# Performance work log

Hardware: AMD Instinct MI355X
Metric: run time of the kernel (lower is better)

The kernel has to match this reference:

```python
import jax, jax.numpy as jnp
import numpy as np

N_CELL = 66
N_SUB = 29934
N = N_CELL + N_SUB  # 30000 nodes
F = 256
E_HALF = 480000
K = 3
LAYERS = 2
BN_EPS = 1e-5


def setup_inputs() -> dict:
    key = jax.random.key(0)
    ks = jax.random.split(key, 8)
    cell_feat = jax.random.normal(ks[0], (N_CELL, F), dtype=jnp.float32)
    sub_feat = jax.random.normal(ks[1], (N_SUB, F), dtype=jnp.float32)
    # interaction_edge builds a symmetric directed edge list: (a,b) and (b,a)
    src = jax.random.randint(ks[2], (E_HALF,), 0, N)
    dst = jax.random.randint(ks[3], (E_HALF,), 0, N)
    edge_index = jnp.stack([jnp.concatenate([src, dst]),
                            jnp.concatenate([dst, src])], axis=0)
    ew_half = jax.random.uniform(ks[4], (E_HALF,), dtype=jnp.float32, minval=0.1, maxval=1.0)
    edge_weight = jnp.concatenate([ew_half, ew_half])
    glorot = np.sqrt(6.0 / (F + F))
    W1 = jax.random.uniform(ks[5], (F, F), dtype=jnp.float32, minval=-glorot, maxval=glorot)
    W2 = jax.random.uniform(ks[6], (F, F), dtype=jnp.float32, minval=-glorot, maxval=glorot)
    b1 = jnp.zeros((F,), jnp.float32)
    b2 = jnp.zeros((F,), jnp.float32)
    prelu_w = jnp.full((F,), 0.25, jnp.float32)  # PReLU default init
    gamma = jnp.ones((F,), jnp.float32)
    beta = jnp.zeros((F,), jnp.float32)
    return {"cell_feat": cell_feat, "sub_feat": sub_feat,
            "edge_index": edge_index, "edge_weight": edge_weight,
            "W1": W1, "b1": b1, "W2": W2, "b2": b2,
            "prelu_w": prelu_w, "gamma": gamma, "beta": beta}


def _gcn_norm(edge_index, edge_weight, n):
    # SGConv's gcn_norm: add self-loops (weight 1), symmetric degree normalization
    loop = jnp.arange(n)
    row = jnp.concatenate([edge_index[0], loop])  # source j
    col = jnp.concatenate([edge_index[1], loop])  # target i
    ew = jnp.concatenate([edge_weight, jnp.ones((n,), edge_weight.dtype)])
    deg = jax.ops.segment_sum(ew, col, num_segments=n)
    dinv = jnp.where(deg > 0, jax.lax.rsqrt(deg), 0.0)
    norm = dinv[row] * ew * dinv[col]
    return row, col, norm


def _sgconv(x, row, col, norm, W, b, n):
    # K-hop propagation: x <- A_hat^K x, then linear
    for _ in range(K):
        x = jax.ops.segment_sum(norm[:, None] * x[row], col, num_segments=n)
    return x @ W.T + b


def _prelu_bn(x, prelu_w, gamma, beta):
    x = jnp.where(x >= 0, x, prelu_w * x)
    mean = jnp.mean(x, axis=0)
    var = jnp.mean(jnp.square(x - mean), axis=0)  # biased, training-mode BN
    return gamma * (x - mean) * jax.lax.rsqrt(var + BN_EPS) + beta


def reference(cell_feat, sub_feat, edge_index, edge_weight,
              W1, b1, W2, b2, prelu_w, gamma, beta):
    x = jnp.concatenate([cell_feat, sub_feat], axis=0)  # [N, F]
    n = x.shape[0]
    row, col, norm = _gcn_norm(edge_index, edge_weight, n)
    for W, b in ((W1, b1), (W2, b2)):
        x = _sgconv(x, row, col, norm, W, b, n)
        x = _prelu_bn(x, prelu_w, gamma, beta)
    return x[:N_CELL, :], x[N_CELL:, :]
```

## Files before the change

kernel.cpp:

```cpp
#include <hip/hip_runtime.h>
#include <hip/hip_bf16.h>

constexpr int NN    = 30000;
constexpr int NCELL = 66;
constexpr int NF    = 256;
constexpr int CAP   = 80;
constexpr float EPS = 1e-5f;

using bf16x8 = __attribute__((ext_vector_type(8))) short;
using f32x4  = __attribute__((ext_vector_type(4))) float;
using f32x2  = __attribute__((ext_vector_type(2))) float;

__device__ __forceinline__ float bf2f(unsigned short u) {
    return __uint_as_float(((unsigned)u) << 16);
}
__device__ __forceinline__ unsigned short f2bf(float f) {
    __hip_bfloat16 h = __float2bfloat16(f);
    return *reinterpret_cast<unsigned short*>(&h);
}
__device__ __forceinline__ void acc8v(f32x2* acc, float4 u, float w) {
    unsigned a = __float_as_uint(u.x), b = __float_as_uint(u.y);
    unsigned c = __float_as_uint(u.z), d = __float_as_uint(u.w);
    f32x2 wv; wv[0] = w; wv[1] = w;
    f32x2 e0; e0[0] = __uint_as_float(a << 16); e0[1] = __uint_as_float(a & 0xffff0000u);
    f32x2 e1; e1[0] = __uint_as_float(b << 16); e1[1] = __uint_as_float(b & 0xffff0000u);
    f32x2 e2; e2[0] = __uint_as_float(c << 16); e2[1] = __uint_as_float(c & 0xffff0000u);
    f32x2 e3; e3[0] = __uint_as_float(d << 16); e3[1] = __uint_as_float(d & 0xffff0000u);
    acc[0] += wv * e0;
    acc[1] += wv * e1;
    acc[2] += wv * e2;
    acc[3] += wv * e3;
}
__device__ __forceinline__ void acc8(float* acc, float4 u, float w) {
    unsigned a = __float_as_uint(u.x), b = __float_as_uint(u.y);
    unsigned c = __float_as_uint(u.z), d = __float_as_uint(u.w);
    acc[0] += w * __uint_as_float(a << 16);
    acc[1] += w * __uint_as_float(a & 0xffff0000u);
    acc[2] += w * __uint_as_float(b << 16);
    acc[3] += w * __uint_as_float(b & 0xffff0000u);
    acc[4] += w * __uint_as_float(c << 16);
    acc[5] += w * __uint_as_float(c & 0xffff0000u);
    acc[6] += w * __uint_as_float(d << 16);
    acc[7] += w * __uint_as_float(d & 0xffff0000u);
}
__device__ __forceinline__ void edge_meta(const unsigned* p, int& r, float& w) {
    unsigned v = *p;
    r = (int)(v & 0xffffu);
    w = (float)(v >> 16) * (1.0f / 65536.0f);
}

__global__ void k_init(int* fill, float* sums) {
    int i = blockIdx.x * 256 + threadIdx.x;
    if (i < NN) fill[i] = 0;
    if (i < 2 * NF) sums[i] = 0.0f;
}

__global__ void k_zero_stats(float* sums) {
    int i = threadIdx.x;
    if (i < 2 * NF) sums[i] = 0.0f;
}

__global__ void k_cvtw(const float4* __restrict__ W, ushort4* __restrict__ Wh) {
    int idx = blockIdx.x * 256 + threadIdx.x;
    if (idx >= NF * NF / 4) return;
    float4 v = W[idx];
    ushort4 o;
    o.x = f2bf(v.x); o.y = f2bf(v.y); o.z = f2bf(v.z); o.w = f2bf(v.w);
    Wh[idx] = o;
}

__global__ void k_scatter(const int* __restrict__ ei, const float* __restrict__ ew,
                          int* fill, unsigned* __restrict__ bkt, int E) {
    int e = blockIdx.x * 256 + threadIdx.x;
    if (e >= E) return;
    int row = ei[e];
    int col = ei[E + e];
    unsigned q = (unsigned)(ew[e] * 65536.0f);
    int pos = atomicAdd(&fill[col], 1);
    unsigned v = ((unsigned)row) | (q << 16);
    __builtin_nontemporal_store(v, &bkt[(size_t)col * CAP + pos]);
}

__global__ void k_deg(const unsigned* __restrict__ bkt, const int* __restrict__ fill,
                      float* __restrict__ s1, float* __restrict__ s2) {
    int i = blockIdx.x * 256 + threadIdx.x;
    if (i >= NN) return;
    int cnt = fill[i];
    unsigned sq = 0;
    const unsigned* p = bkt + (size_t)i * CAP;
    for (int e = 0; e < cnt; e++) sq += (p[e] >> 16);
    float deg = 1.0f + (float)sq * (1.0f / 65536.0f);
    float di = rsqrtf(deg);
    s2[i] = di;
    s1[i] = di * di;
}

__global__ void k_concat_h(const float4* __restrict__ cell, const float4* __restrict__ sub,
                           const float* __restrict__ dinv, ushort4* __restrict__ xh) {
    int idx = blockIdx.x * 256 + threadIdx.x;
    if (idx >= NN * (NF / 4)) return;
    const int CELL4 = NCELL * (NF / 4);
    float4 v = (idx < CELL4) ? cell[idx] : sub[idx - CELL4];
    float di = dinv[idx >> 6];
    ushort4 o;
    o.x = f2bf(v.x * di); o.y = f2bf(v.y * di);
    o.z = f2bf(v.z * di); o.w = f2bf(v.w * di);
    xh[idx] = o;
}

__global__ __launch_bounds__(256) void k_prop(const ushort* __restrict__ xin,
                                              ushort* __restrict__ xout,
                                              const int* __restrict__ fill,
                                              const unsigned* __restrict__ bkt,
                                              const float* __restrict__ scale) {
    int n = blockIdx.x * 4 + (threadIdx.x >> 6);
    int lane = threadIdx.x & 63;
    int half = lane >> 5;
    int fb = lane & 31;
    const float4* xrow = (const float4*)xin;
    const unsigned* base = bkt + (size_t)n * CAP;
    int cnt = fill[n];
    float4 uself = xrow[n * 32 + fb];
    float sc = scale[n];
    f32x2 acc[4];
    #pragma unroll
    for (int i = 0; i < 4; i++) { acc[i][0] = 0.f; acc[i][1] = 0.f; }
    int steps = cnt >> 1;
    int it = 0;
    int e = half;
    if (8 <= steps) {
        unsigned m[8];
        #pragma unroll
        for (int j = 0; j < 8; j++) m[j] = base[e + 2 * j];
        for (;;) {
            int   r[8];
            float w[8];
            #pragma unroll
            for (int j = 0; j < 8; j++) {
                r[j] = (int)(m[j] & 0xffffu);
                w[j] = (float)(m[j] >> 16) * (1.0f / 65536.0f);
            }
            float4 u[8];
            #pragma unroll
            for (int j = 0; j < 8; j++) u[j] = xrow[r[j] * 32 + fb];
            it += 8; e += 16;
            bool more = (it + 8 <= steps);
            if (more) {
                #pragma unroll
                for (int j = 0; j < 8; j++) m[j] = base[e + 2 * j];
            }
            #pragma unroll
            for (int j = 0; j < 8; j++) acc8v(acc, u[j], w[j]);
            if (!more) break;
        }
    }
    for (; it + 4 <= steps; it += 4, e += 8) {
        int r0, r1, r2, r3; float w0, w1, w2, w3;
        edge_meta(base + e,     r0, w0);
        edge_meta(base + e + 2, r1, w1);
        edge_meta(base + e + 4, r2, w2);
        edge_meta(base + e + 6, r3, w3);
        float4 u0 = xrow[r0 * 32 + fb];
        float4 u1 = xrow[r1 * 32 + fb];
        float4 u2 = xrow[r2 * 32 + fb];
        float4 u3 = xrow[r3 * 32 + fb];
        acc8v(acc, u0, w0); acc8v(acc, u1, w1); acc8v(acc, u2, w2); acc8v(acc, u3, w3);
    }
    for (; it < steps; ++it, e += 2) {
        int r0; float w0;
        edge_meta(base + e, r0, w0);
        float4 u0 = xrow[r0 * 32 + fb];
        acc8v(acc, u0, w0);
    }
    if ((cnt & 1) && half == 0) {
        int r0; float w0;
        edge_meta(base + cnt - 1, r0, w0);
        float4 u0 = xrow[r0 * 32 + fb];
        acc8v(acc, u0, w0);
    }
    float accs[8];
    #pragma unroll
    for (int i = 0; i < 4; i++) { accs[2 * i] = acc[i][0]; accs[2 * i + 1] = acc[i][1]; }
    #pragma unroll
    for (int i = 0; i < 8; i++) accs[i] += __shfl_xor(accs[i], 32);
    if (half == 0) {
        acc8(accs, uself, 1.0f);
        #pragma unroll
        for (int i = 0; i < 8; i++) accs[i] *= sc;
        unsigned p0 = ((unsigned)f2bf(accs[1]) << 16) | f2bf(accs[0]);
        unsigned p1 = ((unsigned)f2bf(accs[3]) << 16) | f2bf(accs[2]);
        unsigned p2 = ((unsigned)f2bf(accs[5]) << 16) | f2bf(accs[4]);
        unsigned p3 = ((unsigned)f2bf(accs[7]) << 16) | f2bf(accs[6]);
        float4 o;
        o.x = __uint_as_float(p0); o.y = __uint_as_float(p1);
        o.z = __uint_as_float(p2); o.w = __uint_as_float(p3);
        ((float4*)xout)[n * 32 + fb] = o;
    }
}

__global__ __launch_bounds__(256) void k_gemm_fused(const short* __restrict__ A,
                                                    const short* __restrict__ B,
                                                    const float* __restrict__ bias,
                                                    const float* __restrict__ pw,
                                                    float* __restrict__ y,
                                                    float* __restrict__ sums) {
    constexpr int RT = NN / 16;
    int w    = threadIdx.x >> 6;
    int lane = threadIdx.x & 63;
    int rt   = blockIdx.x * 4 + w;
    int ml   = lane & 15;
    int q    = lane >> 4;
    bool valid = rt < RT;
    __shared__ float red[2][4][NF];
    f32x4 acc[16];
    #pragma unroll
    for (int i = 0; i < 16; i++) acc[i] = (f32x4){0.f, 0.f, 0.f, 0.f};
    if (valid) {
        const short* arow = A + (rt * 16 + ml) * NF + q * 8;
        #pragma unroll
        for (int ks = 0; ks < 8; ks++) {
            bf16x8 a = *(const bf16x8*)(arow + ks * 32);
            #pragma unroll
            for (int nt = 0; nt < 16; nt++) {
                bf16x8 b = *(const bf16x8*)(B + (nt * 16 + ml) * NF + ks * 32 + q * 8);
                acc[nt] = __builtin_amdgcn_mfma_f32_16x16x32_bf16(a, b, acc[nt], 0, 0, 0);
            }
        }
    }
    #pragma unroll
    for (int nt = 0; nt < 16; nt++) {
        int col = nt * 16 + ml;
        float s = 0.f, s2 = 0.f;
        if (valid) {
            float bb = bias[col];
            float pc = pw[col];
            #pragma unroll
            for (int r = 0; r < 4; r++) {
                float v = acc[nt][r] + bb;
                v = (v >= 0.f) ? v : pc * v;
                s += v; s2 += v * v;
                y[(rt * 16 + q * 4 + r) * NF + col] = v;
            }
        }
        s  += __shfl_xor(s, 16);  s  += __shfl_xor(s, 32);
        s2 += __shfl_xor(s2, 16); s2 += __shfl_xor(s2, 32);
        if (lane < 16) { red[0][w][col] = s; red[1][w][col] = s2; }
    }
    __syncthreads();
    int t = threadIdx.x;
    float v0 = red[0][0][t] + red[0][1][t] + red[0][2][t] + red[0][3][t];
    float v1 = red[1][0][t] + red[1][1][t] + red[1][2][t] + red[1][3][t];
    atomicAdd(&sums[t], v0);
    atomicAdd(&sums[NF + t], v1);
}

__global__ void k_finalize(const float* __restrict__ sums, const float* __restrict__ gamma,
                           const float* __restrict__ beta, float* __restrict__ ss) {
    int t = threadIdx.x;
    float mean = sums[t] / (float)NN;
    float var = sums[NF + t] / (float)NN - mean * mean;
    if (var < 0.f) var = 0.f;
    float istd = rsqrtf(var + EPS);
    float sc = gamma[t] * istd;
    ss[t] = sc;
    ss[NF + t] = beta[t] - mean * sc;
}

__global__ void k_apply_h(const float4* __restrict__ y, const float* __restrict__ ss,
                          const float* __restrict__ dinv, ushort4* __restrict__ xh) {
    int idx = blockIdx.x * 256 + threadIdx.x;
    if (idx >= NN * (NF / 4)) return;
    int f = (idx & 63) * 4;
    float di = dinv[idx >> 6];
    float4 v = y[idx];
    ushort4 o;
    o.x = f2bf((v.x * ss[f]     + ss[NF + f])     * di);
    o.y = f2bf((v.y * ss[f + 1] + ss[NF + f + 1]) * di);
    o.z = f2bf((v.z * ss[f + 2] + ss[NF + f + 2]) * di);
    o.w = f2bf((v.w * ss[f + 3] + ss[NF + f + 3]) * di);
    xh[idx] = o;
}

__global__ void k_apply_out(const float4* __restrict__ y, const float* __restrict__ ss,
                            float4* __restrict__ out) {
    int idx = blockIdx.x * 256 + threadIdx.x;
    if (idx >= NN * (NF / 4)) return;
    int f = (idx & 63) * 4;
    float4 v = y[idx];
    float4 o;
    o.x = v.x * ss[f]     + ss[NF + f];
    o.y = v.y * ss[f + 1] + ss[NF + f + 1];
    o.z = v.z * ss[f + 2] + ss[NF + f + 2];
    o.w = v.w * ss[f + 3] + ss[NF + f + 3];
    out[idx] = o;
}

extern "C" void kernel_launch(void* const* d_in, const int* in_sizes, int n_in,
                              void* d_out, int out_size, void* d_ws, size_t ws_size,
                              hipStream_t stream) {
    const float* cell  = (const float*)d_in[0];
    const float* sub   = (const float*)d_in[1];
    const int*   ei    = (const int*)  d_in[2];
    const float* ew    = (const float*)d_in[3];
    const float* W1    = (const float*)d_in[4];
    const float* bias1 = (const float*)d_in[5];
    const float* W2    = (const float*)d_in[6];
    const float* bias2 = (const float*)d_in[7];
    const float* pw    = (const float*)d_in[8];
    const float* gamma = (const float*)d_in[9];
    const float* beta  = (const float*)d_in[10];
    float* out = (float*)d_out;
    const int E = in_sizes[3];

    char* ws = (char*)d_ws;
    size_t off = 0;
    auto alloc = [&](size_t bytes) -> void* {
        void* p = ws + off;
        off = (off + bytes + 255) & ~((size_t)255);
        return p;
    };
    ushort*   xh0  = (ushort*)  alloc((size_t)NN * NF * 2);
    ushort*   xh1  = (ushort*)  alloc((size_t)NN * NF * 2);
    float*    yf   = (float*)   alloc((size_t)NN * NF * 4);
    ushort*   W1h  = (ushort*)  alloc((size_t)NF * NF * 2);
    ushort*   W2h  = (ushort*)  alloc((size_t)NF * NF * 2);
    unsigned* bkt  = (unsigned*)alloc((size_t)NN * CAP * 4);
    int*      fill = (int*)     alloc((size_t)NN * 4);
    float*    s1   = (float*)   alloc((size_t)NN * 4);
    float*    s2   = (float*)   alloc((size_t)NN * 4);
    float*    sums = (float*)   alloc((size_t)2 * NF * 4);
    float*    ss   = (float*)   alloc((size_t)2 * NF * 4);

    const int gN  = (NN + 255) / 256;
    const int gE  = (E + 255) / 256;
    const int gV4 = (NN * NF / 4 + 255) / 256;
    const int gW4 = (NF * NF / 4 + 255) / 256;
    const int gP  = NN / 4;
    const int gG  = (NN / 16 + 3) / 4;

    k_init<<<gN, 256, 0, stream>>>(fill, sums);
    k_cvtw<<<gW4, 256, 0, stream>>>((const float4*)W1, (ushort4*)W1h);
    k_cvtw<<<gW4, 256, 0, stream>>>((const float4*)W2, (ushort4*)W2h);
    k_scatter<<<gE, 256, 0, stream>>>(ei, ew, fill, bkt, E);
    k_deg<<<gN, 256, 0, stream>>>(bkt, fill, s1, s2);
    k_concat_h<<<gV4, 256, 0, stream>>>((const float4*)cell, (const float4*)sub, s2, (ushort4*)xh0);

    k_prop<<<gP, 256, 0, stream>>>(xh0, xh1, fill, bkt, s1);
    k_prop<<<gP, 256, 0, stream>>>(xh1, xh0, fill, bkt, s1);
    k_prop<<<gP, 256, 0, stream>>>(xh0, xh1, fill, bkt, s2);
    k_gemm_fused<<<gG, 256, 0, stream>>>((const short*)xh1, (const short*)W1h, bias1, pw, yf, sums);
    k_finalize<<<1, 256, 0, stream>>>(sums, gamma, beta, ss);
    k_apply_h<<<gV4, 256, 0, stream>>>((const float4*)yf, ss, s2, (ushort4*)xh0);
    k_zero_stats<<<1, 512, 0, stream>>>(sums);

    k_prop<<<gP, 256, 0, stream>>>(xh0, xh1, fill, bkt, s1);
    k_prop<<<gP, 256, 0, stream>>>(xh1, xh0, fill, bkt, s1);
    k_prop<<<gP, 256, 0, stream>>>(xh0, xh1, fill, bkt, s2);
    k_gemm_fused<<<gG, 256, 0, stream>>>((const short*)xh1, (const short*)W2h, bias2, pw, yf, sums);
    k_finalize<<<1, 256, 0, stream>>>(sums, gamma, beta, ss);
    k_apply_out<<<gV4, 256, 0, stream>>>((const float4*)yf, ss, (float4*)out);
}
```

Measured before the change: 654.0 us.

## Merge setup kernels, partition edge scatter by destination range, fold BN finalize

After: 624.2 us. -4.6%, faster.

```diff
diff --git a/kernel.cpp b/kernel.cpp
--- a/kernel.cpp
+++ b/kernel.cpp
@@ -11,9 +11,6 @@
 using f32x4  = __attribute__((ext_vector_type(4))) float;
 using f32x2  = __attribute__((ext_vector_type(2))) float;
 
-__device__ __forceinline__ float bf2f(unsigned short u) {
-    return __uint_as_float(((unsigned)u) << 16);
-}
 __device__ __forceinline__ unsigned short f2bf(float f) {
     __hip_bfloat16 h = __float2bfloat16(f);
     return *reinterpret_cast<unsigned short*>(&h);
@@ -48,11 +45,35 @@
     r = (int)(v & 0xffffu);
     w = (float)(v >> 16) * (1.0f / 65536.0f);
 }
-
-__global__ void k_init(int* fill, float* sums) {
-    int i = blockIdx.x * 256 + threadIdx.x;
-    if (i < NN) fill[i] = 0;
-    if (i < 2 * NF) sums[i] = 0.0f;
+__device__ __forceinline__ void bn_ss(const float* sums, const float* gamma,
+                                      const float* beta, int col, float& sc, float& sh) {
+    float mean = sums[col] * (1.0f / (float)NN);
+    float var  = sums[NF + col] * (1.0f / (float)NN) - mean * mean;
+    if (var < 0.f) var = 0.f;
+    float istd = rsqrtf(var + EPS);
+    sc = gamma[col] * istd;
+    sh = beta[col] - mean * sc;
+}
+
+__global__ void k_setup(int* fill, float* sums,
+                        const float4* __restrict__ W1, ushort4* __restrict__ W1h,
+                        const float4* __restrict__ W2, ushort4* __restrict__ W2h) {
+    int b = blockIdx.x;
+    if (b < 118) {
+        int i = b * 256 + threadIdx.x;
+        if (i < NN) fill[i] = 0;
+        if (i < 2 * NF) sums[i] = 0.0f;
+    } else {
+        const float4* src = (b < 182) ? W1 : W2;
+        ushort4* dst      = (b < 182) ? W1h : W2h;
+        int idx = (b - ((b < 182) ? 118 : 182)) * 256 + threadIdx.x;
+        if (idx < NF * NF / 4) {
+            float4 v = src[idx];
+            ushort4 o;
+            o.x = f2bf(v.x); o.y = f2bf(v.y); o.z = f2bf(v.z); o.w = f2bf(v.w);
+            dst[idx] = o;
+        }
+    }
 }
 
 __global__ void k_zero_stats(float* sums) {
@@ -60,25 +81,27 @@
     if (i < 2 * NF) sums[i] = 0.0f;
 }
 
-__global__ void k_cvtw(const float4* __restrict__ W, ushort4* __restrict__ Wh) {
-    int idx = blockIdx.x * 256 + threadIdx.x;
-    if (idx >= NF * NF / 4) return;
-    float4 v = W[idx];
-    ushort4 o;
-    o.x = f2bf(v.x); o.y = f2bf(v.y); o.z = f2bf(v.z); o.w = f2bf(v.w);
-    Wh[idx] = o;
-}
-
-__global__ void k_scatter(const int* __restrict__ ei, const float* __restrict__ ew,
-                          int* fill, unsigned* __restrict__ bkt, int E) {
-    int e = blockIdx.x * 256 + threadIdx.x;
-    if (e >= E) return;
-    int row = ei[e];
-    int col = ei[E + e];
-    unsigned q = (unsigned)(ew[e] * 65536.0f);
-    int pos = atomicAdd(&fill[col], 1);
-    unsigned v = ((unsigned)row) | (q << 16);
-    __builtin_nontemporal_store(v, &bkt[(size_t)col * CAP + pos]);
+constexpr int SLICE = 2048;
+__global__ __launch_bounds__(256) void k_scatter8(const int* __restrict__ ei,
+                                                  const float* __restrict__ ew,
+                                                  int* fill, unsigned* __restrict__ bkt,
+                                                  int E) {
+    int r  = blockIdx.x & 7;
+    int s  = blockIdx.x >> 3;
+    int lo = r * (NN / 8);
+    int hi = lo + (NN / 8);
+    int e0 = s * SLICE;
+    int e1 = e0 + SLICE; if (e1 > E) e1 = E;
+    for (int e = e0 + threadIdx.x; e < e1; e += 256) {
+        int col = ei[E + e];
+        if (col >= lo && col < hi) {
+            int row  = ei[e];
+            float wv = ew[e];
+            unsigned q = (unsigned)(wv * 65536.0f);
+            int pos = atomicAdd(&fill[col], 1);
+            bkt[(size_t)col * CAP + pos] = ((unsigned)row) | (q << 16);
+        }
+    }
 }
 
 __global__ void k_deg(const unsigned* __restrict__ bkt, const int* __restrict__ fill,
@@ -254,44 +277,44 @@
     atomicAdd(&sums[NF + t], v1);
 }
 
-__global__ void k_finalize(const float* __restrict__ sums, const float* __restrict__ gamma,
-                           const float* __restrict__ beta, float* __restrict__ ss) {
-    int t = threadIdx.x;
-    float mean = sums[t] / (float)NN;
-    float var = sums[NF + t] / (float)NN - mean * mean;
-    if (var < 0.f) var = 0.f;
-    float istd = rsqrtf(var + EPS);
-    float sc = gamma[t] * istd;
-    ss[t] = sc;
-    ss[NF + t] = beta[t] - mean * sc;
-}
-
-__global__ void k_apply_h(const float4* __restrict__ y, const float* __restrict__ ss,
+__global__ void k_apply_h(const float4* __restrict__ y, const float* __restrict__ sums,
+                          const float* __restrict__ gamma, const float* __restrict__ beta,
                           const float* __restrict__ dinv, ushort4* __restrict__ xh) {
     int idx = blockIdx.x * 256 + threadIdx.x;
     if (idx >= NN * (NF / 4)) return;
     int f = (idx & 63) * 4;
+    float sc0, sh0, sc1, sh1, sc2, sh2, sc3, sh3;
+    bn_ss(sums, gamma, beta, f,     sc0, sh0);
+    bn_ss(sums, gamma, beta, f + 1, sc1, sh1);
+    bn_ss(sums, gamma, beta, f + 2, sc2, sh2);
+    bn_ss(sums, gamma, beta, f + 3, sc3, sh3);
     float di = dinv[idx >> 6];
     float4 v = y[idx];
     ushort4 o;
-    o.x = f2bf((v.x * ss[f]     + ss[NF + f])     * di);
-    o.y = f2bf((v.y * ss[f + 1] + ss[NF + f + 1]) * di);
-    o.z = f2bf((v.z * ss[f + 2] + ss[NF + f + 2]) * di);
-    o.w = f2bf((v.w * ss[f + 3] + ss[NF + f + 3]) * di);
+    o.x = f2bf((v.x * sc0 + sh0) * di);
+    o.y = f2bf((v.y * sc1 + sh1) * di);
+    o.z = f2bf((v.z * sc2 + sh2) * di);
+    o.w = f2bf((v.w * sc3 + sh3) * di);
     xh[idx] = o;
 }
 
-__global__ void k_apply_out(const float4* __restrict__ y, const float* __restrict__ ss,
+__global__ void k_apply_out(const float4* __restrict__ y, const float* __restrict__ sums,
+                            const float* __restrict__ gamma, const float* __restrict__ beta,
                             float4* __restrict__ out) {
     int idx = blockIdx.x * 256 + threadIdx.x;
     if (idx >= NN * (NF / 4)) return;
     int f = (idx & 63) * 4;
+    float sc0, sh0, sc1, sh1, sc2, sh2, sc3, sh3;
+    bn_ss(sums, gamma, beta, f,     sc0, sh0);
+    bn_ss(sums, gamma, beta, f + 1, sc1, sh1);
+    bn_ss(sums, gamma, beta, f + 2, sc2, sh2);
+    bn_ss(sums, gamma, beta, f + 3, sc3, sh3);
     float4 v = y[idx];
     float4 o;
-    o.x = v.x * ss[f]     + ss[NF + f];
-    o.y = v.y * ss[f + 1] + ss[NF + f + 1];
-    o.z = v.z * ss[f + 2] + ss[NF + f + 2];
-    o.w = v.w * ss[f + 3] + ss[NF + f + 3];
+    o.x = v.x * sc0 + sh0;
+    o.y = v.y * sc1 + sh1;
+    o.z = v.z * sc2 + sh2;
+    o.w = v.w * sc3 + sh3;
     out[idx] = o;
 }
 
@@ -329,19 +352,17 @@
     float*    s1   = (float*)   alloc((size_t)NN * 4);
     float*    s2   = (float*)   alloc((size_t)NN * 4);
     float*    sums = (float*)   alloc((size_t)2 * NF * 4);
-    float*    ss   = (float*)   alloc((size_t)2 * NF * 4);
 
     const int gN  = (NN + 255) / 256;
-    const int gE  = (E + 255) / 256;
+    const int gSU = 118 + 64 + 64;
+    const int gS8 = ((E + SLICE - 1) / SLICE) * 8;
     const int gV4 = (NN * NF / 4 + 255) / 256;
-    const int gW4 = (NF * NF / 4 + 255) / 256;
     const int gP  = NN / 4;
     const int gG  = (NN / 16 + 3) / 4;
 
-    k_init<<<gN, 256, 0, stream>>>(fill, sums);
-    k_cvtw<<<gW4, 256, 0, stream>>>((const float4*)W1, (ushort4*)W1h);
-    k_cvtw<<<gW4, 256, 0, stream>>>((const float4*)W2, (ushort4*)W2h);
-    k_scatter<<<gE, 256, 0, stream>>>(ei, ew, fill, bkt, E);
+    k_setup<<<gSU, 256, 0, stream>>>(fill, sums, (const float4*)W1, (ushort4*)W1h,
+                                     (const float4*)W2, (ushort4*)W2h);
+    k_scatter8<<<gS8, 256, 0, stream>>>(ei, ew, fill, bkt, E);
     k_deg<<<gN, 256, 0, stream>>>(bkt, fill, s1, s2);
     k_concat_h<<<gV4, 256, 0, stream>>>((const float4*)cell, (const float4*)sub, s2, (ushort4*)xh0);
 
@@ -349,14 +370,12 @@
     k_prop<<<gP, 256, 0, stream>>>(xh1, xh0, fill, bkt, s1);
     k_prop<<<gP, 256, 0, stream>>>(xh0, xh1, fill, bkt, s2);
     k_gemm_fused<<<gG, 256, 0, stream>>>((const short*)xh1, (const short*)W1h, bias1, pw, yf, sums);
-    k_finalize<<<1, 256, 0, stream>>>(sums, gamma, beta, ss);
-    k_apply_h<<<gV4, 256, 0, stream>>>((const float4*)yf, ss, s2, (ushort4*)xh0);
+    k_apply_h<<<gV4, 256, 0, stream>>>((const float4*)yf, sums, gamma, beta, s2, (ushort4*)xh0);
     k_zero_stats<<<1, 512, 0, stream>>>(sums);
 
     k_prop<<<gP, 256, 0, stream>>>(xh0, xh1, fill, bkt, s1);
     k_prop<<<gP, 256, 0, stream>>>(xh1, xh0, fill, bkt, s1);
     k_prop<<<gP, 256, 0, stream>>>(xh0, xh1, fill, bkt, s2);
     k_gemm_fused<<<gG, 256, 0, stream>>>((const short*)xh1, (const short*)W2h, bias2, pw, yf, sums);
-    k_finalize<<<1, 256, 0, stream>>>(sums, gamma, beta, ss);
-    k_apply_out<<<gV4, 256, 0, stream>>>((const float4*)yf, ss, (float4*)out);
-}
+    k_apply_out<<<gV4, 256, 0, stream>>>((const float4*)yf, sums, gamma, beta, (float4*)out);
+}
```
